# Kernel tuning notes

Measured on AMD Instinct MI355X. Metric: run time of the kernel, lower is better.

## Reference

```python
import jax, jax.numpy as jnp
import numpy as np

N = 3  # lateral kernel size (hardcoded in original call via i:i+3 slices)


def _center_zero_mask(n, dtype):
    # ones everywhere except the center tap (the layer excludes self-connection)
    m = jnp.ones((n, n), dtype=dtype)
    return m.at[n // 2, n // 2].set(0.0)


def setup_inputs() -> dict:
    key = jax.random.key(0)
    kx, kk = jax.random.split(key)
    B, H, W, C = 32, 56, 56, 256
    x = jax.random.normal(kx, (B, H, W, C), dtype=jnp.float32)
    # glorot-ish scale for a (3,3,C) depthwise kernel
    kernel = jax.random.normal(kk, (N, N, C), dtype=jnp.float32) * 0.1
    return {"x": x, "kernel": kernel}


def reference(x, kernel):
    # x: [B,H,W,C], kernel: [n,n,C] (one n x n filter per channel)
    n, _, ch = kernel.shape
    masked = kernel * _center_zero_mask(n, kernel.dtype)[:, :, None]  # zero center tap
    # depthwise conv: HWIO with I=1, feature_group_count=C
    w = masked.reshape(n, n, 1, ch)
    out = jax.lax.conv_general_dilated(
        x, w,
        window_strides=(1, 1),
        padding="SAME",
        dimension_numbers=("NHWC", "HWIO", "NHWC"),
        feature_group_count=ch,
    )
    return out + x  # residual add
```

## Files before the change

### kernel.cpp

```cpp
#include <hip/hip_runtime.h>


#define BB 32
#define HH 56
#define WW 56
#define CC 256
#define C4 (CC / 4)

__global__ __launch_bounds__(256) void contour_kernel(
    const float4* __restrict__ x,
    const float4* __restrict__ kern,
    float4* __restrict__ out)
{
    int idx = blockIdx.x * blockDim.x + threadIdx.x;
    int c4 = idx & (C4 - 1);
    int t  = idx >> 6;
    int w  = t % WW;
    t /= WW;
    int h  = t % HH;
    int b  = t / HH;
    if (b >= BB) return;

    int base = idx;
    float4 ctr = x[base];
    float4 acc = ctr;

    #pragma unroll
    for (int ky = 0; ky < 3; ++ky) {
        int hh = h + ky - 1;
        if (hh < 0 || hh >= HH) continue;
        #pragma unroll
        for (int kx = 0; kx < 3; ++kx) {
            if (ky == 1 && kx == 1) continue;
            int ww = w + kx - 1;
            if (ww < 0 || ww >= WW) continue;
            float4 xv = x[((b * HH + hh) * WW + ww) * C4 + c4];
            float4 kv = kern[(ky * 3 + kx) * C4 + c4];
            acc.x += xv.x * kv.x;
            acc.y += xv.y * kv.y;
            acc.z += xv.z * kv.z;
            acc.w += xv.w * kv.w;
        }
    }
    out[base] = acc;
}

extern "C" void kernel_launch(void* const* d_in, const int* in_sizes, int n_in,
                              void* d_out, int out_size, void* d_ws, size_t ws_size,
                              hipStream_t stream) {
    const float4* x    = (const float4*)d_in[0];
    const float4* kern = (const float4*)d_in[1];
    float4* out        = (float4*)d_out;

    const int total = BB * HH * WW * C4;
    const int block = 256;
    const int grid  = (total + block - 1) / block;
    contour_kernel<<<grid, block, 0, stream>>>(x, kern, out);
}
```

Baseline: 214.2 us.

## Compute four output columns per thread with register sliding window and XCD remap

```diff
diff --git a/kernel.cpp b/kernel.cpp
--- a/kernel.cpp
+++ b/kernel.cpp
@@ -4,45 +4,66 @@
 #define BB 32
 #define HH 56
 #define WW 56
-#define CC 256
-#define C4 (CC / 4)
+#define C4 64
+#define NXCD 8
+#define WG 14
 
 __global__ __launch_bounds__(256) void contour_kernel(
     const float4* __restrict__ x,
     const float4* __restrict__ kern,
     float4* __restrict__ out)
 {
-    int idx = blockIdx.x * blockDim.x + threadIdx.x;
-    int c4 = idx & (C4 - 1);
-    int t  = idx >> 6;
-    int w  = t % WW;
-    t /= WW;
-    int h  = t % HH;
-    int b  = t / HH;
-    if (b >= BB) return;
+    const int per_xcd = gridDim.x / NXCD;
+    const int blk = (blockIdx.x % NXCD) * per_xcd + blockIdx.x / NXCD;
 
-    int base = idx;
-    float4 ctr = x[base];
-    float4 acc = ctr;
+    const int tid = threadIdx.x;
+    const int c4  = tid & 63;
+    const int wi  = blk * 4 + (tid >> 6);
+    const int g   = wi % WG;
+    const int h   = (wi / WG) % HH;
+    const int b   = wi / (WG * HH);
+    const int w0  = g * 4;
 
+    float4 kv[3][3];
     #pragma unroll
-    for (int ky = 0; ky < 3; ++ky) {
-        int hh = h + ky - 1;
-        if (hh < 0 || hh >= HH) continue;
+    for (int r = 0; r < 3; ++r)
         #pragma unroll
-        for (int kx = 0; kx < 3; ++kx) {
-            if (ky == 1 && kx == 1) continue;
-            int ww = w + kx - 1;
-            if (ww < 0 || ww >= WW) continue;
-            float4 xv = x[((b * HH + hh) * WW + ww) * C4 + c4];
-            float4 kv = kern[(ky * 3 + kx) * C4 + c4];
-            acc.x += xv.x * kv.x;
-            acc.y += xv.y * kv.y;
-            acc.z += xv.z * kv.z;
-            acc.w += xv.w * kv.w;
+        for (int c = 0; c < 3; ++c)
+            kv[r][c] = kern[(r * 3 + c) * C4 + c4];
+
+    const float4 zero = make_float4(0.f, 0.f, 0.f, 0.f);
+    float4 win[3][6];
+    #pragma unroll
+    for (int r = 0; r < 3; ++r) {
+        const int hh = h - 1 + r;
+        const bool hok = (hh >= 0) && (hh < HH);
+        const int rowbase = (b * HH + hh) * WW;
+        #pragma unroll
+        for (int c = 0; c < 6; ++c) {
+            const int ww = w0 - 1 + c;
+            const bool ok = hok && (ww >= 0) && (ww < WW);
+            win[r][c] = ok ? x[(rowbase + ww) * C4 + c4] : zero;
         }
     }
-    out[base] = acc;
+
+    const int obase = ((b * HH + h) * WW + w0) * C4 + c4;
+    #pragma unroll
+    for (int j = 0; j < 4; ++j) {
+        float4 acc = win[1][j + 1];
+        #pragma unroll
+        for (int r = 0; r < 3; ++r)
+            #pragma unroll
+            for (int c = 0; c < 3; ++c) {
+                if (r == 1 && c == 1) continue;
+                const float4 xv = win[r][j + c];
+                const float4 kk = kv[r][c];
+                acc.x += xv.x * kk.x;
+                acc.y += xv.y * kk.y;
+                acc.z += xv.z * kk.z;
+                acc.w += xv.w * kk.w;
+            }
+        out[obase + j * C4] = acc;
+    }
 }
 
 extern "C" void kernel_launch(void* const* d_in, const int* in_sizes, int n_in,
@@ -52,8 +73,8 @@
     const float4* kern = (const float4*)d_in[1];
     float4* out        = (float4*)d_out;
 
-    const int total = BB * HH * WW * C4;
+    const int waves = BB * HH * WG;
     const int block = 256;
-    const int grid  = (total + block - 1) / block;
+    const int grid  = waves / 4;
     contour_kernel<<<grid, block, 0, stream>>>(x, kern, out);
 }
```

New measurement: 245.0 us. 1.14x slower.
